# Kernel optimization log

Measured on AMD Instinct MI355X. Metric: run time of the kernel, lower is better.

Reference implementation:

```python
import jax, jax.numpy as jnp
import numpy as np


def setup_inputs() -> dict:
    key = jax.random.key(0)
    N, K, F, N_UP = 400000, 5, 128, 100000
    k1, k2, k3, k4 = jax.random.split(key, 4)
    features = jax.random.normal(k1, (N, F), dtype=jnp.float32)
    weights_down = jax.random.uniform(k2, (N, K), dtype=jnp.float32)
    nidx_down = jax.random.randint(k3, (N, K), 0, N).astype(jnp.int32)
    sel_idx_up = jax.random.randint(k4, (N_UP, 1), 0, N).astype(jnp.int32)
    return {
        "features": features,
        "weights_down": weights_down,
        "nidx_down": nidx_down,
        "sel_idx_up": sel_idx_up,
    }


def reference(features, weights_down, nidx_down, sel_idx_up):
    # PushUp(mode='mean', add_self=False), weight=None, nweights=None
    N, F = features.shape
    dt = features.dtype
    # mode == 'mean' and weight is None -> prepend a ones weight column
    ones_w = jnp.ones((N, 1), dtype=dt)
    up_f = jnp.concatenate([ones_w, features], axis=-1)          # [N, F+1]

    # push_sum: each node i pushes nweights[i,k] * up_f[i] into row nidx[i,k];
    # nidx < 0 means "no neighbor" and is skipped.
    valid = nidx_down >= 0                                        # [N, K]
    idx = jnp.where(valid, nidx_down, 0)                          # [N, K]
    contrib = jnp.where(valid[:, :, None],
                        weights_down[:, :, None] * up_f[:, None, :],
                        jnp.zeros((), dt))                        # [N, K, F+1]
    pushed = jnp.zeros((N, F + 1), dtype=dt).at[idx.reshape(-1)].add(
        contrib.reshape(-1, F + 1))                               # [N, F+1]

    # gather_nd with [N_up,1] indices == row gather
    sel = pushed[sel_idx_up[:, 0]]                                # [N_up, F+1]

    # mean normalization: clamp weight-sum, divide_no_nan
    wsum = jax.nn.relu(sel[:, 0:1])
    wsum = jnp.where(wsum > 0.0, wsum, jnp.asarray(0.001, dt))
    out = jnp.where(wsum != 0.0, sel[:, 1:] / wsum, jnp.zeros((), dt))
    return out.reshape(-1, F)
```

## Files before the change

### kernel.cpp

```cpp
#include <hip/hip_runtime.h>

#define BLOCK 256
#define CAP 24

typedef float f2v __attribute__((ext_vector_type(2)));
typedef int   i4v __attribute__((ext_vector_type(4)));
typedef float f4v __attribute__((ext_vector_type(4)));

__global__ void mark_kernel(const int* __restrict__ sel, unsigned int* __restrict__ bits,
                            int n_up) {
    int u = blockIdx.x * blockDim.x + threadIdx.x;
    if (u < n_up) {
        int v = sel[u];
        atomicOr(&bits[v >> 5], 1u << (v & 31));
    }
}

template <int KK>
__global__ void fill_kernel(const int* __restrict__ nidx, const float* __restrict__ wdown,
                            const unsigned int* __restrict__ bits,
                            int* __restrict__ cursor, int2* __restrict__ slots, int E) {
    int i4 = blockIdx.x * blockDim.x + threadIdx.x;
    int base = i4 * 4;
    if (base + 3 < E) {
        i4v mm = __builtin_nontemporal_load((const i4v*)nidx + i4);
        f4v ww = __builtin_nontemporal_load((const f4v*)wdown + i4);
        unsigned int b0 = (mm[0] >= 0) ? bits[mm[0] >> 5] : 0u;
        unsigned int b1 = (mm[1] >= 0) ? bits[mm[1] >> 5] : 0u;
        unsigned int b2 = (mm[2] >= 0) ? bits[mm[2] >> 5] : 0u;
        unsigned int b3 = (mm[3] >= 0) ? bits[mm[3] >> 5] : 0u;
        {
            int m = mm[0];
            if ((b0 >> (m & 31)) & 1u) {
                int n = (base + 0) / KK;
                int c = atomicAdd(&cursor[m], 1);
                if (c < CAP) slots[(size_t)m * CAP + c] = make_int2(n, __float_as_int(ww[0]));
            }
        }
        {
            int m = mm[1];
            if ((b1 >> (m & 31)) & 1u) {
                int n = (base + 1) / KK;
                int c = atomicAdd(&cursor[m], 1);
                if (c < CAP) slots[(size_t)m * CAP + c] = make_int2(n, __float_as_int(ww[1]));
            }
        }
        {
            int m = mm[2];
            if ((b2 >> (m & 31)) & 1u) {
                int n = (base + 2) / KK;
                int c = atomicAdd(&cursor[m], 1);
                if (c < CAP) slots[(size_t)m * CAP + c] = make_int2(n, __float_as_int(ww[2]));
            }
        }
        {
            int m = mm[3];
            if ((b3 >> (m & 31)) & 1u) {
                int n = (base + 3) / KK;
                int c = atomicAdd(&cursor[m], 1);
                if (c < CAP) slots[(size_t)m * CAP + c] = make_int2(n, __float_as_int(ww[3]));
            }
        }
    } else if (base < E) {
        for (int e = base; e < E; ++e) {
            int m = nidx[e];
            if (m >= 0 && ((bits[m >> 5] >> (m & 31)) & 1u)) {
                int n = e / KK;
                int c = atomicAdd(&cursor[m], 1);
                if (c < CAP) slots[(size_t)m * CAP + c] = make_int2(n, __float_as_int(wdown[e]));
            }
        }
    }
}

__global__ void fill_generic_kernel(const int* __restrict__ nidx, const float* __restrict__ wdown,
                                    const unsigned int* __restrict__ bits,
                                    int* __restrict__ cursor, int2* __restrict__ slots,
                                    int E, int K) {
    int e = blockIdx.x * blockDim.x + threadIdx.x;
    if (e >= E) return;
    int m = nidx[e];
    if (m >= 0 && ((bits[m >> 5] >> (m & 31)) & 1u)) {
        int n = e / K;
        int c = atomicAdd(&cursor[m], 1);
        if (c < CAP) slots[(size_t)m * CAP + c] = make_int2(n, __float_as_int(wdown[e]));
    }
}

__global__ __launch_bounds__(256, 8)
void gather_kernel(const float2* __restrict__ feat2, const int2* __restrict__ slots,
                   const int* __restrict__ cursor, const int* __restrict__ sel,
                   float2* __restrict__ out2, int n_up) {
    int gid = blockIdx.x * blockDim.x + threadIdx.x;
    int r = __builtin_amdgcn_readfirstlane(gid >> 6);
    int l = threadIdx.x & 63;
    if (r >= n_up) return;

    int m = __builtin_amdgcn_readfirstlane(sel[r]);
    const int2* __restrict__ srow = slots + (size_t)m * CAP;

    int deg = cursor[m];
    int nn0[8];
    float w0[8];
#pragma unroll
    for (int t = 0; t < 8; ++t) {
        int2 pr = srow[t];
        nn0[t] = pr.x;
        w0[t] = __int_as_float(pr.y);
    }
    if (deg > CAP) deg = CAP;

    float2 acc = make_float2(0.f, 0.f);
    float ws = 0.f;

    {
        int c = deg < 8 ? deg : 8;
        float2 f[8];
#pragma unroll
        for (int t = 0; t < 8; ++t)
            if (t < c) f[t] = feat2[(size_t)nn0[t] * 64 + l];
#pragma unroll
        for (int t = 0; t < 8; ++t)
            if (t < c) {
                acc.x = fmaf(w0[t], f[t].x, acc.x);
                acc.y = fmaf(w0[t], f[t].y, acc.y);
                ws += w0[t];
            }
    }

    for (int j = 8; j < deg; j += 8) {
        int c = deg - j;
        if (c > 8) c = 8;
        int nn[8];
        float w[8];
#pragma unroll
        for (int t = 0; t < 8; ++t) {
            int2 pr = srow[j + t];
            nn[t] = pr.x;
            w[t] = __int_as_float(pr.y);
        }
        float2 f[8];
#pragma unroll
        for (int t = 0; t < 8; ++t)
            if (t < c) f[t] = feat2[(size_t)nn[t] * 64 + l];
#pragma unroll
        for (int t = 0; t < 8; ++t)
            if (t < c) {
                acc.x = fmaf(w[t], f[t].x, acc.x);
                acc.y = fmaf(w[t], f[t].y, acc.y);
                ws += w[t];
            }
    }

    float d = (ws > 0.f) ? ws : 0.001f;
    float inv = 1.0f / d;
    f2v o;
    o.x = acc.x * inv;
    o.y = acc.y * inv;
    __builtin_nontemporal_store(o, (f2v*)&out2[(size_t)r * 64 + l]);
}

extern "C" void kernel_launch(void* const* d_in, const int* in_sizes, int n_in,
                              void* d_out, int out_size, void* d_ws, size_t ws_size,
                              hipStream_t stream) {
    const float* features = (const float*)d_in[0];
    const float* wdown    = (const float*)d_in[1];
    const int*   nidx     = (const int*)d_in[2];
    const int*   sel      = (const int*)d_in[3];

    int E    = in_sizes[1];
    int n_up = in_sizes[3];
    int F    = out_size / n_up;
    int N    = in_sizes[0] / F;
    int K    = E / N;

    int Nb = (N + 31) / 32;
    int* cursor = (int*)d_ws;
    unsigned int* bits = (unsigned int*)(cursor + N);
    size_t zero_bytes = (size_t)N * sizeof(int) + (size_t)Nb * sizeof(unsigned int);
    size_t slots_off = (zero_bytes + 15) & ~(size_t)15;
    int2* slots = (int2*)((char*)d_ws + slots_off);

    (void)hipMemsetAsync(d_ws, 0, zero_bytes, stream);

    mark_kernel<<<(n_up + BLOCK - 1) / BLOCK, BLOCK, 0, stream>>>(sel, bits, n_up);

    int e4 = (E + 3) / 4;
    if (K == 5) {
        fill_kernel<5><<<(e4 + BLOCK - 1) / BLOCK, BLOCK, 0, stream>>>(
            nidx, wdown, bits, cursor, slots, E);
    } else {
        fill_generic_kernel<<<(E + BLOCK - 1) / BLOCK, BLOCK, 0, stream>>>(
            nidx, wdown, bits, cursor, slots, E, K);
    }

    long long threads = (long long)n_up * 64;
    gather_kernel<<<(int)((threads + BLOCK - 1) / BLOCK), BLOCK, 0, stream>>>(
        (const float2*)features, slots, cursor, sel, (float2*)d_out, n_up);
}
```

Baseline: 367.4 us.

## Process two output rows per wavefront with float4 feature gathers

The gather kernel now assigns two selected rows to each 64-lane wavefront, with each half-wave using float4 loads to cover the 128-feature row, which halves the wave count and widens the memory accesses. The fill kernel swaps nontemporal vector loads for plain int4/float4 loads, and the output store is no longer nontemporal. In exchange, both halves iterate to the larger of the two degrees, so lanes whose row has fewer neighbours sit idle, and each wave now reads two slot rows.

```diff
diff --git a/kernel.cpp b/kernel.cpp
--- a/kernel.cpp
+++ b/kernel.cpp
@@ -2,10 +2,6 @@
 
 #define BLOCK 256
 #define CAP 24
-
-typedef float f2v __attribute__((ext_vector_type(2)));
-typedef int   i4v __attribute__((ext_vector_type(4)));
-typedef float f4v __attribute__((ext_vector_type(4)));
 
 __global__ void mark_kernel(const int* __restrict__ sel, unsigned int* __restrict__ bits,
                             int n_up) {
@@ -23,42 +19,42 @@
     int i4 = blockIdx.x * blockDim.x + threadIdx.x;
     int base = i4 * 4;
     if (base + 3 < E) {
-        i4v mm = __builtin_nontemporal_load((const i4v*)nidx + i4);
-        f4v ww = __builtin_nontemporal_load((const f4v*)wdown + i4);
-        unsigned int b0 = (mm[0] >= 0) ? bits[mm[0] >> 5] : 0u;
-        unsigned int b1 = (mm[1] >= 0) ? bits[mm[1] >> 5] : 0u;
-        unsigned int b2 = (mm[2] >= 0) ? bits[mm[2] >> 5] : 0u;
-        unsigned int b3 = (mm[3] >= 0) ? bits[mm[3] >> 5] : 0u;
-        {
-            int m = mm[0];
+        int4 mm = ((const int4*)nidx)[i4];
+        float4 ww = ((const float4*)wdown)[i4];
+        unsigned int b0 = (mm.x >= 0) ? bits[mm.x >> 5] : 0u;
+        unsigned int b1 = (mm.y >= 0) ? bits[mm.y >> 5] : 0u;
+        unsigned int b2 = (mm.z >= 0) ? bits[mm.z >> 5] : 0u;
+        unsigned int b3 = (mm.w >= 0) ? bits[mm.w >> 5] : 0u;
+        {
+            int m = mm.x;
             if ((b0 >> (m & 31)) & 1u) {
                 int n = (base + 0) / KK;
                 int c = atomicAdd(&cursor[m], 1);
-                if (c < CAP) slots[(size_t)m * CAP + c] = make_int2(n, __float_as_int(ww[0]));
-            }
-        }
-        {
-            int m = mm[1];
+                if (c < CAP) slots[(size_t)m * CAP + c] = make_int2(n, __float_as_int(ww.x));
+            }
+        }
+        {
+            int m = mm.y;
             if ((b1 >> (m & 31)) & 1u) {
                 int n = (base + 1) / KK;
                 int c = atomicAdd(&cursor[m], 1);
-                if (c < CAP) slots[(size_t)m * CAP + c] = make_int2(n, __float_as_int(ww[1]));
-            }
-        }
-        {
-            int m = mm[2];
+                if (c < CAP) slots[(size_t)m * CAP + c] = make_int2(n, __float_as_int(ww.y));
+            }
+        }
+        {
+            int m = mm.z;
             if ((b2 >> (m & 31)) & 1u) {
                 int n = (base + 2) / KK;
                 int c = atomicAdd(&cursor[m], 1);
-                if (c < CAP) slots[(size_t)m * CAP + c] = make_int2(n, __float_as_int(ww[2]));
-            }
-        }
-        {
-            int m = mm[3];
+                if (c < CAP) slots[(size_t)m * CAP + c] = make_int2(n, __float_as_int(ww.z));
+            }
+        }
+        {
+            int m = mm.w;
             if ((b3 >> (m & 31)) & 1u) {
                 int n = (base + 3) / KK;
                 int c = atomicAdd(&cursor[m], 1);
-                if (c < CAP) slots[(size_t)m * CAP + c] = make_int2(n, __float_as_int(ww[3]));
+                if (c < CAP) slots[(size_t)m * CAP + c] = make_int2(n, __float_as_int(ww.w));
             }
         }
     } else if (base < E) {
@@ -88,76 +84,101 @@
 }
 
 __global__ __launch_bounds__(256, 8)
-void gather_kernel(const float2* __restrict__ feat2, const int2* __restrict__ slots,
+void gather_kernel(const float4* __restrict__ feat4, const int2* __restrict__ slots,
                    const int* __restrict__ cursor, const int* __restrict__ sel,
-                   float2* __restrict__ out2, int n_up) {
+                   float4* __restrict__ out4, int n_up) {
     int gid = blockIdx.x * blockDim.x + threadIdx.x;
-    int r = __builtin_amdgcn_readfirstlane(gid >> 6);
-    int l = threadIdx.x & 63;
-    if (r >= n_up) return;
-
-    int m = __builtin_amdgcn_readfirstlane(sel[r]);
-    const int2* __restrict__ srow = slots + (size_t)m * CAP;
-
-    int deg = cursor[m];
-    int nn0[8];
-    float w0[8];
+    int wid = gid >> 6;
+    int lane = threadIdx.x & 63;
+    int half = lane >> 5;
+    int l = lane & 31;
+    int rA = wid * 2;
+    if (rA >= n_up) return;
+    int hasB = (rA + 1 < n_up);
+    int rB = hasB ? rA + 1 : rA;
+
+    int mA = __builtin_amdgcn_readfirstlane(sel[rA]);
+    int mB = __builtin_amdgcn_readfirstlane(sel[rB]);
+    const int2* __restrict__ srA = slots + (size_t)mA * CAP;
+    const int2* __restrict__ srB = slots + (size_t)mB * CAP;
+
+    int degA = cursor[mA];
+    int degB = cursor[mB];
+    int nnA[8], nnB[8];
+    float wA[8], wB[8];
 #pragma unroll
     for (int t = 0; t < 8; ++t) {
-        int2 pr = srow[t];
-        nn0[t] = pr.x;
-        w0[t] = __int_as_float(pr.y);
-    }
-    if (deg > CAP) deg = CAP;
-
-    float2 acc = make_float2(0.f, 0.f);
+        int2 a = srA[t];
+        int2 b = srB[t];
+        nnA[t] = a.x; wA[t] = __int_as_float(a.y);
+        nnB[t] = b.x; wB[t] = __int_as_float(b.y);
+    }
+    if (degA > CAP) degA = CAP;
+    if (degB > CAP) degB = CAP;
+    if (!hasB) degB = 0;
+    int deg_v = half ? degB : degA;
+    int degM = degA > degB ? degA : degB;
+
+    float4 acc = make_float4(0.f, 0.f, 0.f, 0.f);
     float ws = 0.f;
 
     {
-        int c = deg < 8 ? deg : 8;
-        float2 f[8];
-#pragma unroll
-        for (int t = 0; t < 8; ++t)
-            if (t < c) f[t] = feat2[(size_t)nn0[t] * 64 + l];
-#pragma unroll
-        for (int t = 0; t < 8; ++t)
-            if (t < c) {
-                acc.x = fmaf(w0[t], f[t].x, acc.x);
-                acc.y = fmaf(w0[t], f[t].y, acc.y);
-                ws += w0[t];
-            }
-    }
-
-    for (int j = 8; j < deg; j += 8) {
-        int c = deg - j;
+        int c = deg_v < 8 ? deg_v : 8;
+        float4 f[8];
+#pragma unroll
+        for (int t = 0; t < 8; ++t)
+            if (t < c) {
+                int nn = half ? nnB[t] : nnA[t];
+                f[t] = feat4[(size_t)nn * 32 + l];
+            }
+#pragma unroll
+        for (int t = 0; t < 8; ++t)
+            if (t < c) {
+                float wt = half ? wB[t] : wA[t];
+                acc.x = fmaf(wt, f[t].x, acc.x);
+                acc.y = fmaf(wt, f[t].y, acc.y);
+                acc.z = fmaf(wt, f[t].z, acc.z);
+                acc.w = fmaf(wt, f[t].w, acc.w);
+                ws += wt;
+            }
+    }
+
+    for (int j = 8; j < degM; j += 8) {
+        int nnA2[8], nnB2[8];
+        float wA2[8], wB2[8];
+#pragma unroll
+        for (int t = 0; t < 8; ++t) {
+            int2 a = srA[j + t];
+            int2 b = srB[j + t];
+            nnA2[t] = a.x; wA2[t] = __int_as_float(a.y);
+            nnB2[t] = b.x; wB2[t] = __int_as_float(b.y);
+        }
+        int c = deg_v - j;
         if (c > 8) c = 8;
-        int nn[8];
-        float w[8];
-#pragma unroll
-        for (int t = 0; t < 8; ++t) {
-            int2 pr = srow[j + t];
-            nn[t] = pr.x;
-            w[t] = __int_as_float(pr.y);
-        }
-        float2 f[8];
-#pragma unroll
-        for (int t = 0; t < 8; ++t)
-            if (t < c) f[t] = feat2[(size_t)nn[t] * 64 + l];
-#pragma unroll
-        for (int t = 0; t < 8; ++t)
-            if (t < c) {
-                acc.x = fmaf(w[t], f[t].x, acc.x);
-                acc.y = fmaf(w[t], f[t].y, acc.y);
-                ws += w[t];
+        float4 f[8];
+#pragma unroll
+        for (int t = 0; t < 8; ++t)
+            if (t < c) {
+                int nn = half ? nnB2[t] : nnA2[t];
+                f[t] = feat4[(size_t)nn * 32 + l];
+            }
+#pragma unroll
+        for (int t = 0; t < 8; ++t)
+            if (t < c) {
+                float wt = half ? wB2[t] : wA2[t];
+                acc.x = fmaf(wt, f[t].x, acc.x);
+                acc.y = fmaf(wt, f[t].y, acc.y);
+                acc.z = fmaf(wt, f[t].z, acc.z);
+                acc.w = fmaf(wt, f[t].w, acc.w);
+                ws += wt;
             }
     }
 
     float d = (ws > 0.f) ? ws : 0.001f;
     float inv = 1.0f / d;
-    f2v o;
-    o.x = acc.x * inv;
-    o.y = acc.y * inv;
-    __builtin_nontemporal_store(o, (f2v*)&out2[(size_t)r * 64 + l]);
+    int r = rA + half;
+    if (r < n_up)
+        out4[(size_t)r * 32 + l] = make_float4(acc.x * inv, acc.y * inv, acc.z * inv, acc.w * inv);
 }
 
 extern "C" void kernel_launch(void* const* d_in, const int* in_sizes, int n_in,
@@ -194,7 +215,8 @@
             nidx, wdown, bits, cursor, slots, E, K);
     }
 
-    long long threads = (long long)n_up * 64;
+    long long waves = (n_up + 1) / 2;
+    long long threads = waves * 64;
     gather_kernel<<<(int)((threads + BLOCK - 1) / BLOCK), BLOCK, 0, stream>>>(
-        (const float2*)features, slots, cursor, sel, (float2*)d_out, n_up);
-}
+        (const float4*)features, slots, cursor, sel, (float4*)d_out, n_up);
+}
```

New measurement: 353.4 us. 3.8% less time.
